# Performance work log

Measured on AMD Instinct MI355X. Metric: run time of the kernel, lower is better.

## Reference

```python
import jax, jax.numpy as jnp
import numpy as np

QLEN, MLEN, BSZ = 1024, 1024, 4
D_MODEL, N_HEAD, D_HEAD, D_INNER = 1024, 16, 64, 4096
KLEN = QLEN + MLEN  # = rlen
LN_EPS = 1e-5


def setup_inputs() -> dict:
    key = jax.random.key(0)
    ks = jax.random.split(key, 16)
    s = 0.02
    nhd = N_HEAD * D_HEAD
    inp = {
        "dec_inp": jax.random.normal(ks[0], (QLEN, BSZ, D_MODEL), jnp.float32),
        "r": jax.random.normal(ks[1], (KLEN, D_MODEL), jnp.float32),
        "r_w_bias": jax.random.normal(ks[2], (N_HEAD, D_HEAD), jnp.float32) * s,
        "r_r_bias": jax.random.normal(ks[3], (N_HEAD, D_HEAD), jnp.float32) * s,
        "mems": jax.random.normal(ks[4], (MLEN, BSZ, D_MODEL), jnp.float32),
        # causal mask with memory: position j visible to query i iff j <= i + MLEN
        "dec_attn_mask": (jnp.arange(KLEN)[None, :] > (jnp.arange(QLEN)[:, None] + MLEN))[:, :, None],
        # parameters
        "qkv_w": jax.random.normal(ks[5], (D_MODEL, 3 * nhd), jnp.float32) * s,
        "r_w": jax.random.normal(ks[6], (D_MODEL, nhd), jnp.float32) * s,
        "o_w": jax.random.normal(ks[7], (nhd, D_MODEL), jnp.float32) * s,
        "ln1_w": jnp.ones((D_MODEL,), jnp.float32),
        "ln1_b": jnp.zeros((D_MODEL,), jnp.float32),
        "ln2_w": jnp.ones((D_MODEL,), jnp.float32),
        "ln2_b": jnp.zeros((D_MODEL,), jnp.float32),
        "ff_w1": jax.random.normal(ks[8], (D_MODEL, D_INNER), jnp.float32) * s,
        "ff_b1": jnp.zeros((D_INNER,), jnp.float32),
        "ff_w2": jax.random.normal(ks[9], (D_INNER, D_MODEL), jnp.float32) * s,
        "ff_b2": jnp.zeros((D_MODEL,), jnp.float32),
    }
    return inp


def _layer_norm(x, w, b):
    mu = jnp.mean(x, axis=-1, keepdims=True)
    var = jnp.mean(jnp.square(x - mu), axis=-1, keepdims=True)
    return (x - mu) * jax.lax.rsqrt(var + LN_EPS) * w + b


def _rel_shift(x):
    # x: [qlen, rlen, bsz, n_head] -- Transformer-XL pad/reshape shift
    q, rl = x.shape[0], x.shape[1]
    zero_pad = jnp.zeros((q, 1) + x.shape[2:], x.dtype)
    x_padded = jnp.concatenate([zero_pad, x], axis=1)
    x_padded = x_padded.reshape((rl + 1, q) + x.shape[2:])
    return x_padded[1:].reshape(x.shape)


def reference(dec_inp, r, r_w_bias, r_r_bias, mems, dec_attn_mask,
              qkv_w, r_w, o_w, ln1_w, ln1_b, ln2_w, ln2_b,
              ff_w1, ff_b1, ff_w2, ff_b2):
    qlen, bsz = dec_inp.shape[0], dec_inp.shape[1]
    nhd = N_HEAD * D_HEAD
    scale = 1.0 / (D_HEAD ** 0.5)

    cat = jnp.concatenate([mems, dec_inp], axis=0)          # [klen, b, d]
    w_heads = cat @ qkv_w                                   # [klen, b, 3*nhd]
    w_head_q, w_head_k, w_head_v = jnp.split(w_heads, 3, axis=-1)
    w_head_q = w_head_q[-qlen:]                             # [qlen, b, nhd]
    klen = w_head_k.shape[0]

    w_head_q = w_head_q.reshape(qlen, bsz, N_HEAD, D_HEAD)
    w_head_k = w_head_k.reshape(klen, bsz, N_HEAD, D_HEAD)
    w_head_v = w_head_v.reshape(klen, bsz, N_HEAD, D_HEAD)
    r_head_k = (r @ r_w).reshape(-1, N_HEAD, D_HEAD)        # [rlen, n, d]

    AC = jnp.einsum('ibnd,jbnd->ijbn', w_head_q + r_w_bias, w_head_k)
    BD = jnp.einsum('ibnd,jnd->ijbn', w_head_q + r_r_bias, r_head_k)
    BD = _rel_shift(BD)

    attn_score = (AC + BD) * scale                          # [q, k, b, n]
    attn_score = jnp.where(dec_attn_mask[:, :, :, None], -jnp.inf, attn_score)
    attn_prob = jax.nn.softmax(attn_score, axis=1)

    attn_vec = jnp.einsum('ijbn,jbnd->ibnd', attn_prob, w_head_v)
    attn_out = attn_vec.reshape(qlen, bsz, nhd) @ o_w       # [q, b, d]

    output = _layer_norm(dec_inp + attn_out, ln1_w, ln1_b)
    ff = jax.nn.relu(output @ ff_w1 + ff_b1) @ ff_w2 + ff_b2
    return _layer_norm(output + ff, ln2_w, ln2_b)
```

## Files before the change

### kernel.cpp

```cpp
#include <hip/hip_runtime.h>
#include <hip/hip_bf16.h>
#include <math.h>

#define QLEN 1024
#define MLEN 1024
#define BSZ 4
#define KLEN 2048
#define NH 16
#define DH 64
#define DM 1024
#define DI 4096
#define NHD 1024
#define LN_EPS 1e-5f

typedef short bf16x8 __attribute__((ext_vector_type(8)));
typedef float f32x4 __attribute__((ext_vector_type(4)));
typedef unsigned int uint4v __attribute__((ext_vector_type(4)));

__device__ __forceinline__ float bf2f(unsigned short u) {
    union { unsigned u32; float f; } x; x.u32 = ((unsigned)u) << 16; return x.f;
}
__device__ __forceinline__ unsigned short f2bf(float f) {
    __hip_bfloat16 h = __float2bfloat16(f);
    return *(unsigned short*)&h;
}

static const size_t OFF_CATB  = 0;
static const size_t OFF_VTG   = 0;
static const size_t OFF_WHB   = 16777216;
static const size_t OFF_RB    = 67108864;
static const size_t OFF_RHKB  = 71303168;
static const size_t OFF_AVB   = 75497472;
static const size_t OFF_TMPB  = 83886080;
static const size_t OFF_ML    = 92274688;
static const size_t OFF_LN1F  = 100663296;
static const size_t OFF_LN1B  = 117440512;
static const size_t OFF_FFHB  = 125829120;
static const size_t OFF_QKVWT = 159383552;
static const size_t OFF_RWT   = 165675008;
static const size_t OFF_OWT   = 167772160;
static const size_t OFF_FFW1T = 169869312;
static const size_t OFF_FFW2T = 178257920;

__global__ __launch_bounds__(256) void cast_cat(const float* __restrict__ mems,
                                                const float* __restrict__ dec,
                                                unsigned short* __restrict__ out) {
    size_t i8 = ((size_t)blockIdx.x * 256 + threadIdx.x) * 8;
    const size_t half = (size_t)MLEN * BSZ * DM;
    const float* src = (i8 < half) ? (mems + i8) : (dec + (i8 - half));
    float4 v0 = *(const float4*)src;
    float4 v1 = *(const float4*)(src + 4);
    ushort4 o0 = {f2bf(v0.x), f2bf(v0.y), f2bf(v0.z), f2bf(v0.w)};
    ushort4 o1 = {f2bf(v1.x), f2bf(v1.y), f2bf(v1.z), f2bf(v1.w)};
    *(ushort4*)&out[i8] = o0;
    *(ushort4*)&out[i8 + 4] = o1;
}

__global__ __launch_bounds__(256) void cast_f32_bf16(const float* __restrict__ in,
                                                     unsigned short* __restrict__ out) {
    size_t i8 = ((size_t)blockIdx.x * 256 + threadIdx.x) * 8;
    float4 v0 = *(const float4*)(in + i8);
    float4 v1 = *(const float4*)(in + i8 + 4);
    ushort4 o0 = {f2bf(v0.x), f2bf(v0.y), f2bf(v0.z), f2bf(v0.w)};
    ushort4 o1 = {f2bf(v1.x), f2bf(v1.y), f2bf(v1.z), f2bf(v1.w)};
    *(ushort4*)&out[i8] = o0;
    *(ushort4*)&out[i8 + 4] = o1;
}

__global__ __launch_bounds__(256) void transpose_cast_all(
        const float* __restrict__ qkv_w, const float* __restrict__ r_w,
        const float* __restrict__ o_w,  const float* __restrict__ ff_w1,
        const float* __restrict__ ff_w2,
        unsigned short* __restrict__ qkvwT, unsigned short* __restrict__ rwT,
        unsigned short* __restrict__ owT, unsigned short* __restrict__ ffw1T,
        unsigned short* __restrict__ ffw2T) {
    __shared__ float tile[32][33];
    const int bid = blockIdx.x;
    const float* in; unsigned short* out; int K, N, nx, lid;
    if (bid < 3072)      { in = qkv_w; out = qkvwT; K = 1024; N = 3072; nx = 96;  lid = bid; }
    else if (bid < 4096) { in = r_w;   out = rwT;   K = 1024; N = 1024; nx = 32;  lid = bid - 3072; }
    else if (bid < 5120) { in = o_w;   out = owT;   K = 1024; N = 1024; nx = 32;  lid = bid - 4096; }
    else if (bid < 9216) { in = ff_w1; out = ffw1T; K = 1024; N = 4096; nx = 128; lid = bid - 5120; }
    else                 { in = ff_w2; out = ffw2T; K = 4096; N = 1024; nx = 32;  lid = bid - 9216; }
    const int n0 = (lid % nx) * 32;
    const int k0 = (lid / nx) * 32;
    const int t = threadIdx.x;
    const int r = t >> 3;
    const int c0 = (t & 7) << 2;
    float4 v = *(const float4*)&in[(size_t)(k0 + r) * N + n0 + c0];
    tile[r][c0 + 0] = v.x; tile[r][c0 + 1] = v.y;
    tile[r][c0 + 2] = v.z; tile[r][c0 + 3] = v.w;
    __syncthreads();
    ushort4 o = {f2bf(tile[c0 + 0][r]), f2bf(tile[c0 + 1][r]),
                 f2bf(tile[c0 + 2][r]), f2bf(tile[c0 + 3][r])};
    *(ushort4*)&out[(size_t)(n0 + r) * K + k0 + c0] = o;
}

__global__ __launch_bounds__(256) void gemm_bf16(const unsigned short* __restrict__ A,
                                                 const unsigned short* __restrict__ Bt,
                                                 const float* __restrict__ bias,
                                                 void* __restrict__ C,
                                                 int M, int N, int K, int flags) {
    __shared__ __align__(16) unsigned short As[128 * 64];
    __shared__ __align__(16) unsigned short Bs[128 * 64];

    const int tid = threadIdx.x;
    const int w = tid >> 6, l = tid & 63;
    const int wr = w >> 1, wc = w & 1;
    const int row0 = blockIdx.y * 128;
    const int col0 = blockIdx.x * 128;

    f32x4 acc[4][4] = {};

    uint4v ra[4], rb[4];
    {
#pragma unroll
        for (int q = 0; q < 4; ++q) {
            int f = q * 256 + tid, r = f >> 3, c = f & 7;
            ra[q] = *(const uint4v*)&A[(size_t)(row0 + r) * K + c * 8];
            rb[q] = *(const uint4v*)&Bt[(size_t)(col0 + r) * K + c * 8];
        }
    }

    const int nt = K >> 6;
    for (int kt = 0; kt < nt; ++kt) {
        __syncthreads();
#pragma unroll
        for (int q = 0; q < 4; ++q) {
            int f = q * 256 + tid, r = f >> 3, c = f & 7;
            int sw = (c ^ (r & 7)) << 3;
            *(uint4v*)&As[r * 64 + sw] = ra[q];
            *(uint4v*)&Bs[r * 64 + sw] = rb[q];
        }
        __syncthreads();
        if (kt + 1 < nt) {
            const int k0 = (kt + 1) << 6;
#pragma unroll
            for (int q = 0; q < 4; ++q) {
                int f = q * 256 + tid, r = f >> 3, c = f & 7;
                ra[q] = *(const uint4v*)&A[(size_t)(row0 + r) * K + k0 + c * 8];
                rb[q] = *(const uint4v*)&Bt[(size_t)(col0 + r) * K + k0 + c * 8];
            }
        }
#pragma unroll
        for (int ks = 0; ks < 2; ++ks) {
            bf16x8 a[4], bfr[4];
#pragma unroll
            for (int m = 0; m < 4; ++m) {
                int arow = wr * 64 + m * 16 + (l & 15);
                int chunk = (ks * 4 + (l >> 4)) ^ (arow & 7);
                a[m] = *(const bf16x8*)&As[arow * 64 + chunk * 8];
            }
#pragma unroll
            for (int n = 0; n < 4; ++n) {
                int brow = wc * 64 + n * 16 + (l & 15);
                int chunk = (ks * 4 + (l >> 4)) ^ (brow & 7);
                bfr[n] = *(const bf16x8*)&Bs[brow * 64 + chunk * 8];
            }
#pragma unroll
            for (int m = 0; m < 4; ++m)
#pragma unroll
                for (int n = 0; n < 4; ++n)
                    acc[m][n] = __builtin_amdgcn_mfma_f32_16x16x32_bf16(a[m], bfr[n], acc[m][n], 0, 0, 0);
        }
    }

#pragma unroll
    for (int n = 0; n < 4; ++n) {
        const int ccol = col0 + wc * 64 + n * 16 + (l & 15);
        const float bv = (flags & 1) ? bias[ccol] : 0.0f;
#pragma unroll
        for (int m = 0; m < 4; ++m) {
            const int crow0 = row0 + wr * 64 + m * 16 + ((l >> 4) << 2);
#pragma unroll
            for (int reg = 0; reg < 4; ++reg) {
                float v = acc[m][n][reg] + bv;
                if (flags & 2) v = fmaxf(v, 0.0f);
                if (flags & 4)
                    ((unsigned short*)C)[(size_t)(crow0 + reg) * N + ccol] = f2bf(v);
                else
                    ((float*)C)[(size_t)(crow0 + reg) * N + ccol] = v;
            }
        }
    }
}

__global__ __launch_bounds__(256) void vtrans(const unsigned short* __restrict__ whb,
                                              unsigned short* __restrict__ vtg) {
    __shared__ unsigned short tile[64][72];
    const int bn = blockIdx.y;
    const int b = bn >> 4, n = bn & 15, nb = n * 64;
    const int jt0 = blockIdx.x * 64;
    const int tid = threadIdx.x;
#pragma unroll
    for (int g = 0; g < 2; ++g) {
        int f = g * 256 + tid;
        int key = f >> 3, c = f & 7;
        uint4v v = *(const uint4v*)&whb[((size_t)(jt0 + key) * 4 + b) * 3072 + 2048 + nb + c * 8];
        *(uint4v*)&tile[key][c * 8] = v;
    }
    __syncthreads();
#pragma unroll
    for (int g = 0; g < 2; ++g) {
        int f = g * 256 + tid;
        int d = f >> 3, ck = f & 7;
        unsigned short tmp[8];
#pragma unroll
        for (int e = 0; e < 8; ++e) tmp[e] = tile[ck * 8 + e][d];
        *(uint4v*)&vtg[(size_t)bn * 131072 + (size_t)d * 2048 + jt0 + ck * 8] = *(uint4v*)tmp;
    }
}

__global__ __launch_bounds__(512) void flash_attn_mfma(const unsigned short* __restrict__ whb,
                                                       const unsigned short* __restrict__ rhkb,
                                                       const unsigned short* __restrict__ vtg,
                                                       const float* __restrict__ r_w_bias,
                                                       const float* __restrict__ r_r_bias,
                                                       float* __restrict__ opart,
                                                       float* __restrict__ ml) {
    const int bid = blockIdx.x;
    const int bn = bid >> 3;
    const int kk0 = bid & 7;
    const int b = bn >> 4, n = bn & 15, nb = n * 64;
    const int tid = threadIdx.x;
    const int wq = tid >> 6;
    const int lane = tid & 63;
    const int rg = lane >> 4;
    const int lc = lane & 15;
    const int m7 = lc & 7;

    __shared__ __align__(16) unsigned short Ks[4096];
    __shared__ __align__(16) unsigned short Rs[16384];
    __shared__ __align__(16) unsigned short Vt[4096];
    __shared__ __align__(16) unsigned short SCR[8][1440];

    const int wbase_off = 112 - 16 * wq;
    const int srow = tid >> 3;
    const int sc = tid & 7;
    unsigned short* scr = &SCR[wq][0];

#pragma unroll 1
    for (int job = 0; job < 2; ++job) {
        const int h = job;
        const int bx = job ? (7 - kk0) : kk0;
        const int i0 = bx << 7;
        const int halfn = bx + 9;
        const int kt0 = h * halfn;
        const int ktend = kt0 + halfn;

        bf16x8 qac0, qac1, qbd0, qbd1;
        {
            const int qrow = MLEN + i0 + wq * 16 + lc;
            const unsigned short* qp = whb + ((size_t)qrow * 4 + b) * 3072 + nb + rg * 8;
            bf16x8 q0 = *(const bf16x8*)(qp);
            bf16x8 q1 = *(const bf16x8*)(qp + 32);
            const float* wbp = r_w_bias + nb + rg * 8;
            const float* rbp = r_r_bias + nb + rg * 8;
#pragma unroll
            for (int e = 0; e < 8; ++e) {
                const float v0 = bf2f((unsigned short)q0[e]);
                const float v1 = bf2f((unsigned short)q1[e]);
                qac0[e] = (short)f2bf((v0 + wbp[e]) * 0.125f);
                qbd0[e] = (short)f2bf((v0 + rbp[e]) * 0.125f);
                qac1[e] = (short)f2bf((v1 + wbp[32 + e]) * 0.125f);
                qbd1[e] = (short)f2bf((v1 + rbp[32 + e]) * 0.125f);
            }
        }

        f32x4 Oacc[4] = {};
        float mrun = -INFINITY, lrun = 0.f;

        uint4v pk, pv, pr3[3];
        {
            const int j0 = kt0 << 6;
            pk = *(const uint4v*)&whb[((size_t)(j0 + srow) * 4 + b) * 3072 + 1024 + nb + sc * 8];
            pv = *(const uint4v*)&vtg[(size_t)bn * 131072 + (size_t)srow * 2048 + j0 + sc * 8];
            const int relst = j0 - i0 + 896;
#pragma unroll
            for (int p = 0; p < 3; ++p) {
                int a = relst + p * 64 + srow;
                if (a > 2047) a = 2047;
                pr3[p] = *(const uint4v*)&rhkb[(size_t)a * 1024 + nb + sc * 8];
            }
        }

        for (int kt = kt0; kt < ktend; ++kt) {
            const int jt0 = kt << 6;
            const int relbase = jt0 - i0 + 896;
            __syncthreads();

            *(uint4v*)&Ks[srow * 64 + ((sc ^ (srow & 7)) << 3)] = pk;
            *(uint4v*)&Vt[srow * 64 + ((sc ^ (srow & 7)) << 3)] = pv;
            if (kt == kt0) {
#pragma unroll
                for (int p = 0; p < 3; ++p) {
                    int a = relbase + p * 64 + srow;
                    if (a > 2047) a = 2047;
                    const int dst = ((a >> 6) & 3) * 4096 + (a & 63) * 64 + ((sc ^ (a & 7)) << 3);
                    *(uint4v*)&Rs[dst] = pr3[p];
                }
            } else {
                int a = relbase + 128 + srow;
                if (a > 2047) a = 2047;
                const int dst = ((a >> 6) & 3) * 4096 + (a & 63) * 64 + ((sc ^ (a & 7)) << 3);
                *(uint4v*)&Rs[dst] = pr3[0];
            }
            if (kt + 1 < ktend) {
                const int jn = jt0 + 64;
                pk = *(const uint4v*)&whb[((size_t)(jn + srow) * 4 + b) * 3072 + 1024 + nb + sc * 8];
                pv = *(const uint4v*)&vtg[(size_t)bn * 131072 + (size_t)srow * 2048 + jn + sc * 8];
                int a = relbase + 192 + srow;
                if (a > 2047) a = 2047;
                pr3[0] = *(const uint4v*)&rhkb[(size_t)a * 1024 + nb + sc * 8];
            }
            __syncthreads();

            f32x4 S[4];
            __builtin_amdgcn_s_setprio(1);
#pragma unroll
            for (int nf = 0; nf < 4; ++nf) {
                const int row = nf * 16 + lc;
                const bf16x8 kf0 = *(const bf16x8*)&Ks[row * 64 + ((rg ^ m7) << 3)];
                const bf16x8 kf1 = *(const bf16x8*)&Ks[row * 64 + (((4 + rg) ^ m7) << 3)];
                f32x4 zz = {0.f, 0.f, 0.f, 0.f};
                zz = __builtin_amdgcn_mfma_f32_16x16x32_bf16(kf0, qac0, zz, 0, 0, 0);
                S[nf] = __builtin_amdgcn_mfma_f32_16x16x32_bf16(kf1, qac1, zz, 0, 0, 0);
            }
            __builtin_amdgcn_s_setprio(0);

            const int wbase = relbase + wbase_off;
#pragma unroll
            for (int g = 0; g < 5; ++g) {
                const int a = wbase + g * 16 + lc;
                const int rbase = ((a >> 6) & 3) * 4096 + (a & 63) * 64;
                const bf16x8 rf0 = *(const bf16x8*)&Rs[rbase + ((rg ^ m7) << 3)];
                const bf16x8 rf1 = *(const bf16x8*)&Rs[rbase + (((4 + rg) ^ m7) << 3)];
                f32x4 bd = {0.f, 0.f, 0.f, 0.f};
                bd = __builtin_amdgcn_mfma_f32_16x16x32_bf16(rf0, qbd0, bd, 0, 0, 0);
                bd = __builtin_amdgcn_mfma_f32_16x16x32_bf16(rf1, qbd1, bd, 0, 0, 0);
                const int wrow = g * 16 + rg * 4;
#pragma unroll
                for (int r = 0; r < 4; ++r)
                    scr[(wrow + r) * 18 + lc] = f2bf(bd[r]);
            }

            const bool needmask = (wbase + 78 > 2047);
            float tmax = -INFINITY;
#pragma unroll
            for (int nf = 0; nf < 4; ++nf) {
#pragma unroll
                for (int r = 0; r < 4; ++r) {
                    const int wb_ = 15 + nf * 16 + rg * 4 + r - lc;
                    float s = S[nf][r] + bf2f(scr[wb_ * 18 + lc]);
                    if (needmask) s = (wbase + wb_ <= 2047) ? s : -INFINITY;
                    S[nf][r] = s;
                    tmax = fmaxf(tmax, s);
                }
            }

            tmax = fmaxf(tmax, __shfl_xor(tmax, 16));
            tmax = fmaxf(tmax, __shfl_xor(tmax, 32));
            const float mn = fmaxf(mrun, tmax);
            const float ef = __expf(mrun - mn);
            mrun = mn;
            float rsum = 0.f;
#pragma unroll
            for (int nf = 0; nf < 4; ++nf) {
#pragma unroll
                for (int r = 0; r < 4; ++r) {
                    const float p = __expf(S[nf][r] - mn);
                    S[nf][r] = p;
                    rsum += p;
                }
            }
            rsum += __shfl_xor(rsum, 16);
            rsum += __shfl_xor(rsum, 32);
            lrun = lrun * ef + rsum;
            if (__any(ef < 1.0f)) {
#pragma unroll
                for (int nf = 0; nf < 4; ++nf)
#pragma unroll
                    for (int r = 0; r < 4; ++r) Oacc[nf][r] *= ef;
            }

#pragma unroll
            for (int nf = 0; nf < 4; ++nf) {
                ushort4 pw = {f2bf(S[nf][0]), f2bf(S[nf][1]), f2bf(S[nf][2]), f2bf(S[nf][3])};
                const int chunk = nf * 2 + (rg >> 1);
                *(ushort4*)&scr[lc * 64 + ((chunk ^ m7) << 3) + ((rg & 1) << 2)] = pw;
            }

            {
                const bf16x8 pf0 = *(const bf16x8*)&scr[lc * 64 + ((rg ^ m7) << 3)];
                const bf16x8 pf1 = *(const bf16x8*)&scr[lc * 64 + (((4 + rg) ^ m7) << 3)];
                __builtin_amdgcn_s_setprio(1);
#pragma unroll
                for (int nf = 0; nf < 4; ++nf) {
                    const int row = nf * 16 + lc;
                    const bf16x8 vf0 = *(const bf16x8*)&Vt[row * 64 + ((rg ^ m7) << 3)];
                    const bf16x8 vf1 = *(const bf16x8*)&Vt[row * 64 + (((4 + rg) ^ m7) << 3)];
                    Oacc[nf] = __builtin_amdgcn_mfma_f32_16x16x32_bf16(vf0, pf0, Oacc[nf], 0, 0, 0);
                    Oacc[nf] = __builtin_amdgcn_mfma_f32_16x16x32_bf16(vf1, pf1, Oacc[nf], 0, 0, 0);
                }
                __builtin_amdgcn_s_setprio(0);
            }
        }

        const int qg = i0 + wq * 16 + lc;
        const int rowf = qg * 4 + b;
        float* op = opart + (size_t)h * 4194304 + (size_t)rowf * 1024 + nb;
#pragma unroll
        for (int nf = 0; nf < 4; ++nf) {
            float4 o = {Oacc[nf][0], Oacc[nf][1], Oacc[nf][2], Oacc[nf][3]};
            *(float4*)&op[nf * 16 + rg * 4] = o;
        }
        if (rg == 0) {
            float* mp = ml + (size_t)h * 131072 + ((size_t)rowf * 16 + n) * 2;
            mp[0] = mrun;
            mp[1] = lrun;
        }
    }
}

__global__ __launch_bounds__(256) void merge_attn(const float* __restrict__ opart,
                                                  const float* __restrict__ ml,
                                                  unsigned short* __restrict__ avb) {
    const size_t g = (size_t)blockIdx.x * 256 + threadIdx.x;
    const size_t c4 = g << 2;
    const int row = (int)(c4 >> 10);
    const int col = (int)(c4 & 1023);
    const int n = col >> 6;
    const size_t mlb = ((size_t)row * 16 + n) * 2;
    const float m1 = ml[mlb], l1 = ml[mlb + 1];
    const float m2 = ml[131072 + mlb], l2 = ml[131072 + mlb + 1];
    const float m = fmaxf(m1, m2);
    const float e1 = __expf(m1 - m), e2 = __expf(m2 - m);
    const float inv = 1.0f / (e1 * l1 + e2 * l2);
    const float s1 = e1 * inv, s2 = e2 * inv;
    const float4 o1 = *(const float4*)&opart[c4];
    const float4 o2 = *(const float4*)&opart[4194304 + c4];
    ushort4 o = {f2bf(o1.x * s1 + o2.x * s2), f2bf(o1.y * s1 + o2.y * s2),
                 f2bf(o1.z * s1 + o2.z * s2), f2bf(o1.w * s1 + o2.w * s2)};
    *(ushort4*)&avb[c4] = o;
}

__global__ __launch_bounds__(256) void add_ln_kernel(const float* __restrict__ a,
                                                     const unsigned short* __restrict__ b,
                                                     const float* __restrict__ w,
                                                     const float* __restrict__ bias,
                                                     float* __restrict__ out,
                                                     unsigned short* __restrict__ out_bf) {
    const int row = blockIdx.x;
    const int t = threadIdx.x;
    const int c0 = t << 2;
    __shared__ float red[256];

    const float4 av = *(const float4*)&a[(size_t)row * DM + c0];
    const ushort4 bu = *(const ushort4*)&b[(size_t)row * DM + c0];
    float x0 = av.x + bf2f(bu.x), x1 = av.y + bf2f(bu.y);
    float x2 = av.z + bf2f(bu.z), x3 = av.w + bf2f(bu.w);

    red[t] = x0 + x1 + x2 + x3;
    __syncthreads();
    for (int off = 128; off > 0; off >>= 1) {
        if (t < off) red[t] += red[t + off];
        __syncthreads();
    }
    const float mu = red[0] * (1.0f / DM);
    __syncthreads();

    const float d0 = x0 - mu, d1 = x1 - mu, d2 = x2 - mu, d3 = x3 - mu;
    red[t] = d0 * d0 + d1 * d1 + d2 * d2 + d3 * d3;
    __syncthreads();
    for (int off = 128; off > 0; off >>= 1) {
        if (t < off) red[t] += red[t + off];
        __syncthreads();
    }
    const float rstd = rsqrtf(red[0] * (1.0f / DM) + LN_EPS);

    const float4 wv = *(const float4*)&w[c0];
    const float4 bsv = *(const float4*)&bias[c0];
    float4 o = {d0 * rstd * wv.x + bsv.x, d1 * rstd * wv.y + bsv.y,
                d2 * rstd * wv.z + bsv.z, d3 * rstd * wv.w + bsv.w};
    *(float4*)&out[(size_t)row * DM + c0] = o;
    if (out_bf) {
        ushort4 ob = {f2bf(o.x), f2bf(o.y), f2bf(o.z), f2bf(o.w)};
        *(ushort4*)&out_bf[(size_t)row * DM + c0] = ob;
    }
}

extern "C" void kernel_launch(void* const* d_in, const int* in_sizes, int n_in,
                              void* d_out, int out_size, void* d_ws, size_t ws_size,
                              hipStream_t stream) {
    const float* dec_inp  = (const float*)d_in[0];
    const float* r        = (const float*)d_in[1];
    const float* r_w_bias = (const float*)d_in[2];
    const float* r_r_bias = (const float*)d_in[3];
    const float* mems     = (const float*)d_in[4];
    const float* qkv_w    = (const float*)d_in[6];
    const float* r_w      = (const float*)d_in[7];
    const float* o_w      = (const float*)d_in[8];
    const float* ln1_w    = (const float*)d_in[9];
    const float* ln1_b    = (const float*)d_in[10];
    const float* ln2_w    = (const float*)d_in[11];
    const float* ln2_b    = (const float*)d_in[12];
    const float* ff_w1    = (const float*)d_in[13];
    const float* ff_b1    = (const float*)d_in[14];
    const float* ff_w2    = (const float*)d_in[15];
    const float* ff_b2    = (const float*)d_in[16];
    float* out = (float*)d_out;
    char* ws = (char*)d_ws;

    unsigned short* catb  = (unsigned short*)(ws + OFF_CATB);
    unsigned short* vtg   = (unsigned short*)(ws + OFF_VTG);
    unsigned short* whb   = (unsigned short*)(ws + OFF_WHB);
    unsigned short* rb    = (unsigned short*)(ws + OFF_RB);
    unsigned short* rhkb  = (unsigned short*)(ws + OFF_RHKB);
    unsigned short* avb   = (unsigned short*)(ws + OFF_AVB);
    unsigned short* tmpb  = (unsigned short*)(ws + OFF_TMPB);
    float*          mlbuf = (float*)(ws + OFF_ML);
    float*          ln1f  = (float*)(ws + OFF_LN1F);
    unsigned short* ln1b  = (unsigned short*)(ws + OFF_LN1B);
    unsigned short* ffhb  = (unsigned short*)(ws + OFF_FFHB);
    float*          opart = (float*)(ws + OFF_FFHB);
    unsigned short* qkvwT = (unsigned short*)(ws + OFF_QKVWT);
    unsigned short* rwT   = (unsigned short*)(ws + OFF_RWT);
    unsigned short* owT   = (unsigned short*)(ws + OFF_OWT);
    unsigned short* ffw1T = (unsigned short*)(ws + OFF_FFW1T);
    unsigned short* ffw2T = (unsigned short*)(ws + OFF_FFW2T);

    cast_cat<<<dim3(4096), 256, 0, stream>>>(mems, dec_inp, catb);
    cast_f32_bf16<<<dim3(1024), 256, 0, stream>>>(r, rb);
    transpose_cast_all<<<dim3(13312), 256, 0, stream>>>(
        qkv_w, r_w, o_w, ff_w1, ff_w2, qkvwT, rwT, owT, ffw1T, ffw2T);

    gemm_bf16<<<dim3(24, 64), 256, 0, stream>>>(catb, qkvwT, nullptr, whb,
                                                KLEN * BSZ, 3 * NHD, DM, 4);
    gemm_bf16<<<dim3(8, 16), 256, 0, stream>>>(rb, rwT, nullptr, rhkb,
                                               KLEN, NHD, DM, 4);

    vtrans<<<dim3(32, 64), 256, 0, stream>>>(whb, vtg);

    flash_attn_mfma<<<dim3(512), 512, 0, stream>>>(
        whb, rhkb, vtg, r_w_bias, r_r_bias, opart, mlbuf);
    merge_attn<<<dim3(4096), 256, 0, stream>>>(opart, mlbuf, avb);

    gemm_bf16<<<dim3(8, 32), 256, 0, stream>>>(avb, owT, nullptr, tmpb,
                                               QLEN * BSZ, DM, NHD, 4);
    add_ln_kernel<<<dim3(QLEN * BSZ), 256, 0, stream>>>(
        dec_inp, tmpb, ln1_w, ln1_b, ln1f, ln1b);
    gemm_bf16<<<dim3(32, 32), 256, 0, stream>>>(ln1b, ffw1T, ff_b1, ffhb,
                                                QLEN * BSZ, DI, DM, 1 | 2 | 4);
    gemm_bf16<<<dim3(8, 32), 256, 0, stream>>>(ffhb, ffw2T, ff_b2, tmpb,
                                               QLEN * BSZ, DM, DI, 1 | 4);
    add_ln_kernel<<<dim3(QLEN * BSZ), 256, 0, stream>>>(
        ln1f, tmpb, ln2_w, ln2_b, out, nullptr);
}
```

Measured before the change: 369.5 us.

## Add 256x128-tile GEMM for QKV and FF1, use exp2 softmax with folded log2e

```diff
diff --git a/kernel.cpp b/kernel.cpp
--- a/kernel.cpp
+++ b/kernel.cpp
@@ -185,6 +185,106 @@
     }
 }
 
+__global__ __launch_bounds__(512, 4) void gemm_bf16_wide(const unsigned short* __restrict__ A,
+                                                         const unsigned short* __restrict__ Bt,
+                                                         const float* __restrict__ bias,
+                                                         void* __restrict__ C,
+                                                         int M, int N, int K, int flags) {
+    __shared__ __align__(16) unsigned short As[256 * 64];
+    __shared__ __align__(16) unsigned short Bs[128 * 64];
+
+    const int tid = threadIdx.x;
+    const int w = tid >> 6, l = tid & 63;
+    const int wr = w >> 1, wc = w & 1;
+    const int row0 = blockIdx.y * 256;
+    const int col0 = blockIdx.x * 128;
+
+    f32x4 acc[4][4] = {};
+
+    uint4v ra[4], rb[2];
+    {
+#pragma unroll
+        for (int q = 0; q < 4; ++q) {
+            int f = q * 512 + tid, r = f >> 3, c = f & 7;
+            ra[q] = *(const uint4v*)&A[(size_t)(row0 + r) * K + c * 8];
+        }
+#pragma unroll
+        for (int q = 0; q < 2; ++q) {
+            int f = q * 512 + tid, r = f >> 3, c = f & 7;
+            rb[q] = *(const uint4v*)&Bt[(size_t)(col0 + r) * K + c * 8];
+        }
+    }
+
+    const int nt = K >> 6;
+    for (int kt = 0; kt < nt; ++kt) {
+        __syncthreads();
+#pragma unroll
+        for (int q = 0; q < 4; ++q) {
+            int f = q * 512 + tid, r = f >> 3, c = f & 7;
+            *(uint4v*)&As[r * 64 + ((c ^ (r & 7)) << 3)] = ra[q];
+        }
+#pragma unroll
+        for (int q = 0; q < 2; ++q) {
+            int f = q * 512 + tid, r = f >> 3, c = f & 7;
+            *(uint4v*)&Bs[r * 64 + ((c ^ (r & 7)) << 3)] = rb[q];
+        }
+        __syncthreads();
+        if (kt + 1 < nt) {
+            const int k0 = (kt + 1) << 6;
+#pragma unroll
+            for (int q = 0; q < 4; ++q) {
+                int f = q * 512 + tid, r = f >> 3, c = f & 7;
+                ra[q] = *(const uint4v*)&A[(size_t)(row0 + r) * K + k0 + c * 8];
+            }
+#pragma unroll
+            for (int q = 0; q < 2; ++q) {
+                int f = q * 512 + tid, r = f >> 3, c = f & 7;
+                rb[q] = *(const uint4v*)&Bt[(size_t)(col0 + r) * K + k0 + c * 8];
+            }
+        }
+#pragma unroll
+        for (int ks = 0; ks < 2; ++ks) {
+            bf16x8 a[4], bfr[4];
+#pragma unroll
+            for (int m = 0; m < 4; ++m) {
+                int arow = wr * 64 + m * 16 + (l & 15);
+                int chunk = (ks * 4 + (l >> 4)) ^ (arow & 7);
+                a[m] = *(const bf16x8*)&As[arow * 64 + chunk * 8];
+            }
+#pragma unroll
+            for (int n = 0; n < 4; ++n) {
+                int brow = wc * 64 + n * 16 + (l & 15);
+                int chunk = (ks * 4 + (l >> 4)) ^ (brow & 7);
+                bfr[n] = *(const bf16x8*)&Bs[brow * 64 + chunk * 8];
+            }
+#pragma unroll
+            for (int m = 0; m < 4; ++m)
+#pragma unroll
+                for (int n = 0; n < 4; ++n)
+                    acc[m][n] = __builtin_amdgcn_mfma_f32_16x16x32_bf16(a[m], bfr[n], acc[m][n], 0, 0, 0);
+        }
+    }
+
+#pragma unroll
+    for (int n = 0; n < 4; ++n) {
+        const int ccol = col0 + wc * 64 + n * 16 + (l & 15);
+        const float bv = (flags & 1) ? bias[ccol] : 0.0f;
+#pragma unroll
+        for (int m = 0; m < 4; ++m) {
+            const int crow0 = row0 + wr * 64 + m * 16 + ((l >> 4) << 2);
+#pragma unroll
+            for (int reg = 0; reg < 4; ++reg) {
+                float v = acc[m][n][reg] + bv;
+                if (flags & 2) v = fmaxf(v, 0.0f);
+                if (flags & 4)
+                    ((unsigned short*)C)[(size_t)(crow0 + reg) * N + ccol] = f2bf(v);
+                else
+                    ((float*)C)[(size_t)(crow0 + reg) * N + ccol] = v;
+            }
+        }
+    }
+}
+
 __global__ __launch_bounds__(256) void vtrans(const unsigned short* __restrict__ whb,
                                               unsigned short* __restrict__ vtg) {
     __shared__ unsigned short tile[64][72];
@@ -228,6 +328,7 @@
     const int rg = lane >> 4;
     const int lc = lane & 15;
     const int m7 = lc & 7;
+    const float QSCALE = 0.125f * 1.44269504089f;
 
     __shared__ __align__(16) unsigned short Ks[4096];
     __shared__ __align__(16) unsigned short Rs[16384];
@@ -260,10 +361,10 @@
             for (int e = 0; e < 8; ++e) {
                 const float v0 = bf2f((unsigned short)q0[e]);
                 const float v1 = bf2f((unsigned short)q1[e]);
-                qac0[e] = (short)f2bf((v0 + wbp[e]) * 0.125f);
-                qbd0[e] = (short)f2bf((v0 + rbp[e]) * 0.125f);
-                qac1[e] = (short)f2bf((v1 + wbp[32 + e]) * 0.125f);
-                qbd1[e] = (short)f2bf((v1 + rbp[32 + e]) * 0.125f);
+                qac0[e] = (short)f2bf((v0 + wbp[e]) * QSCALE);
+                qbd0[e] = (short)f2bf((v0 + rbp[e]) * QSCALE);
+                qac1[e] = (short)f2bf((v1 + wbp[32 + e]) * QSCALE);
+                qbd1[e] = (short)f2bf((v1 + rbp[32 + e]) * QSCALE);
             }
         }
 
@@ -361,14 +462,14 @@
             tmax = fmaxf(tmax, __shfl_xor(tmax, 16));
             tmax = fmaxf(tmax, __shfl_xor(tmax, 32));
             const float mn = fmaxf(mrun, tmax);
-            const float ef = __expf(mrun - mn);
+            const float ef = exp2f(mrun - mn);
             mrun = mn;
             float rsum = 0.f;
 #pragma unroll
             for (int nf = 0; nf < 4; ++nf) {
 #pragma unroll
                 for (int r = 0; r < 4; ++r) {
-                    const float p = __expf(S[nf][r] - mn);
+                    const float p = exp2f(S[nf][r] - mn);
                     S[nf][r] = p;
                     rsum += p;
                 }
@@ -434,7 +535,7 @@
     const float m1 = ml[mlb], l1 = ml[mlb + 1];
     const float m2 = ml[131072 + mlb], l2 = ml[131072 + mlb + 1];
     const float m = fmaxf(m1, m2);
-    const float e1 = __expf(m1 - m), e2 = __expf(m2 - m);
+    const float e1 = exp2f(m1 - m), e2 = exp2f(m2 - m);
     const float inv = 1.0f / (e1 * l1 + e2 * l2);
     const float s1 = e1 * inv, s2 = e2 * inv;
     const float4 o1 = *(const float4*)&opart[c4];
@@ -534,8 +635,8 @@
     transpose_cast_all<<<dim3(13312), 256, 0, stream>>>(
         qkv_w, r_w, o_w, ff_w1, ff_w2, qkvwT, rwT, owT, ffw1T, ffw2T);
 
-    gemm_bf16<<<dim3(24, 64), 256, 0, stream>>>(catb, qkvwT, nullptr, whb,
-                                                KLEN * BSZ, 3 * NHD, DM, 4);
+    gemm_bf16_wide<<<dim3(24, 32), 512, 0, stream>>>(catb, qkvwT, nullptr, whb,
+                                                     KLEN * BSZ, 3 * NHD, DM, 4);
     gemm_bf16<<<dim3(8, 16), 256, 0, stream>>>(rb, rwT, nullptr, rhkb,
                                                KLEN, NHD, DM, 4);
 
@@ -549,8 +650,8 @@
                                                QLEN * BSZ, DM, NHD, 4);
     add_ln_kernel<<<dim3(QLEN * BSZ), 256, 0, stream>>>(
         dec_inp, tmpb, ln1_w, ln1_b, ln1f, ln1b);
-    gemm_bf16<<<dim3(32, 32), 256, 0, stream>>>(ln1b, ffw1T, ff_b1, ffhb,
-                                                QLEN * BSZ, DI, DM, 1 | 2 | 4);
+    gemm_bf16_wide<<<dim3(32, 16), 512, 0, stream>>>(ln1b, ffw1T, ff_b1, ffhb,
+                                                     QLEN * BSZ, DI, DM, 1 | 2 | 4);
     gemm_bf16<<<dim3(8, 32), 256, 0, stream>>>(ffhb, ffw2T, ff_b2, tmpb,
                                                QLEN * BSZ, DM, DI, 1 | 4);
     add_ln_kernel<<<dim3(QLEN * BSZ), 256, 0, stream>>>(
```

Result: slower. 433.2 us (+17.2%).
